# Optimization experiments

Measured on AMD Instinct MI355X. Metric: run time of the kernel, lower is better.

## Reference

```python
import jax, jax.numpy as jnp
import numpy as np
from jax import lax

B, TZ, TT = 16, 2048, 512
D, DFF, L, V, HEADS = 256, 1024, 6, 512, 4
CH, HID, K, FLOWS, G = 256, 256, 5, 4, 256
PAD_ID = 0
NEG = -1e9
SCALE = 0.02


def setup_inputs():
    key = jax.random.key(0)
    ks = jax.random.split(key, 20)
    n = lambda i, shape, s=SCALE: jax.random.normal(ks[i], shape, jnp.float32) * s
    return {
        'z': jax.random.normal(ks[0], (B, TZ, CH), jnp.float32),
        'text': jax.random.randint(ks[1], (B, TT), 1, V),  # low=1 so no pad tokens
        'cond': jax.random.normal(ks[2], (B, G), jnp.float32),
        'embed': n(3, (V, D), 1.0),
        'wq': n(4, (L, D, D)), 'wk': n(5, (L, D, D)), 'wv': n(6, (L, D, D)), 'wo': n(7, (L, D, D)),
        'bq': jnp.zeros((L, D)), 'bk': jnp.zeros((L, D)), 'bv': jnp.zeros((L, D)), 'bo': jnp.zeros((L, D)),
        'ln1_g': jnp.ones((L, D)), 'ln1_b': jnp.zeros((L, D)),
        'ln2_g': jnp.ones((L, D)), 'ln2_b': jnp.zeros((L, D)),
        'w1': n(8, (L, D, DFF)), 'b1': jnp.zeros((L, DFF)),
        'w2': n(9, (L, DFF, D)), 'b2': jnp.zeros((L, D)),
        'mu_w': n(10, (D, D)), 'mu_b': jnp.zeros((D,)),
        'lv_w': n(11, (D, D)), 'lv_b': jnp.zeros((D,)),
        'flow_in': n(12, (FLOWS, CH // 2, HID)), 'flow_in_b': jnp.zeros((FLOWS, HID)),
        'flow_cond': n(13, (FLOWS, G, HID)),
        'flow_conv': n(14, (FLOWS, K, HID, HID)), 'flow_conv_b': jnp.zeros((FLOWS, HID)),
        'flow_out': n(15, (FLOWS, HID, CH // 2)), 'flow_out_b': jnp.zeros((FLOWS, CH // 2)),
    }


def _pos_encoding(length, d):
    pos = np.arange(length)[:, None].astype(np.float32)
    i = np.arange(d)[None, :]
    angle = pos / np.power(10000.0, (2 * (i // 2)) / d)
    pe = np.where(i % 2 == 0, np.sin(angle), np.cos(angle))
    return jnp.asarray(pe, jnp.float32)


def _ln(x, g, b):
    m = jnp.mean(x, -1, keepdims=True)
    v = jnp.var(x, -1, keepdims=True)
    return g * (x - m) * lax.rsqrt(v + 1e-6) + b


def _mha(x, wq, wk, wv, wo, bq, bk, bv, bo, bias):
    Bq, T, _ = x.shape
    dh = D // HEADS
    heads = lambda y: y.reshape(Bq, T, HEADS, dh).transpose(0, 2, 1, 3)
    q, k, v = heads(x @ wq + bq), heads(x @ wk + bk), heads(x @ wv + bv)
    scores = jnp.einsum('bhqd,bhkd->bhqk', q, k) / jnp.sqrt(jnp.float32(dh)) + bias
    attn = jax.nn.softmax(scores, axis=-1)
    out = jnp.einsum('bhqk,bhkd->bhqd', attn, v).transpose(0, 2, 1, 3).reshape(Bq, T, D)
    return out @ wo + bo


def _mas_path(logp, text_mask):
    # Viterbi monotonic alignment: each latent frame t maps to text index j(t),
    # j nondecreasing with steps in {0, 1}, start at 0, end at last valid token.
    Bq, Tz, Tt = logp.shape
    Q0 = jnp.where(jnp.arange(Tt) == 0, logp[:, 0, :], NEG)

    def fwd(Q, lt):
        Qs = jnp.concatenate([jnp.full((Bq, 1), NEG, Q.dtype), Q[:, :-1]], axis=1)
        return lt + jnp.maximum(Q, Qs), Qs > Q  # choice True => came from j-1

    _, choices = lax.scan(fwd, Q0, jnp.swapaxes(logp, 0, 1)[1:])  # [Tz-1,B,Tt]
    j_last = jnp.sum(text_mask, axis=1).astype(jnp.int32) - 1

    def bwd(j, ch):
        c = jnp.take_along_axis(ch, j[:, None], axis=1)[:, 0]
        jp = j - c.astype(jnp.int32)
        return jp, jp

    _, path_rev = lax.scan(bwd, j_last, choices[::-1])
    path = jnp.concatenate([path_rev[::-1], j_last[None]], axis=0)  # [Tz,B]
    return jnp.swapaxes(path, 0, 1)


def _forward(z, text, cond, embed, wq, wk, wv, wo, bq, bk, bv, bo, ln1_g, ln1_b, ln2_g, ln2_b,
             w1, b1, w2, b2, mu_w, mu_b, lv_w, lv_b,
             flow_in, flow_in_b, flow_cond, flow_conv, flow_conv_b, flow_out, flow_out_b):
    text_mask = text != PAD_ID  # [B,TT]
    bias = jnp.where(text_mask[:, None, None, :], 0.0, NEG)
    # text encoder: scaled embedding + sinusoidal PE + post-LN transformer blocks
    h = embed[text] * jnp.sqrt(jnp.float32(D)) + _pos_encoding(TT, D)[None]
    for l in range(L):
        h = _ln(h + _mha(h, wq[l], wk[l], wv[l], wo[l], bq[l], bk[l], bv[l], bo[l], bias), ln1_g[l], ln1_b[l])
        ffn = jax.nn.relu(h @ w1[l] + b1[l]) @ w2[l] + b2[l]
        h = _ln(h + ffn, ln2_g[l], ln2_b[l])
    mu = h @ mu_w + mu_b
    logvar = h @ lv_w + lv_b
    # residual coupling flows (mean-only, conditioned on global vector)
    zc = z
    for f in range(FLOWS):
        x0, x1 = jnp.split(zc, 2, axis=-1)
        hh = x0 @ flow_in[f] + flow_in_b[f] + (cond @ flow_cond[f])[:, None, :]
        hh = jnp.tanh(lax.conv_general_dilated(hh, flow_conv[f], (1,), 'SAME', rhs_dilation=(1,),
                                               dimension_numbers=('NWC', 'WIO', 'NWC')) + flow_conv_b[f])
        m = hh @ flow_out[f] + flow_out_b[f]
        zc = jnp.concatenate([x1 + m, x0], axis=-1)  # coupling + flip
    # gaussian log-likelihood between latent frames and text distributions
    spr = jnp.exp(-logvar)  # [B,TT,D]
    nc1 = jnp.sum(-0.5 * jnp.log(2.0 * jnp.pi) - 0.5 * logvar, axis=-1)  # [B,TT]
    nc2 = jnp.einsum('btd,bjd->btj', -0.5 * zc * zc, spr)
    nc3 = jnp.einsum('btd,bjd->btj', zc, mu * spr)
    nc4 = jnp.sum(-0.5 * mu * mu * spr, axis=-1)  # [B,TT]
    logp = nc1[:, None, :] + nc2 + nc3 + nc4[:, None, :]  # [B,TZ,TT]
    logp = jnp.where(text_mask[:, None, :], logp, NEG)
    path = _mas_path(logp, text_mask)  # [B,TZ] int32
    ctx = mu[jnp.arange(B)[:, None], path]  # expand text mu along latent time
    return ctx, h


def reference(z, text, cond, embed, wq, wk, wv, wo, bq, bk, bv, bo, ln1_g, ln1_b, ln2_g, ln2_b,
              w1, b1, w2, b2, mu_w, mu_b, lv_w, lv_b,
              flow_in, flow_in_b, flow_cond, flow_conv, flow_conv_b, flow_out, flow_out_b):
    return _forward(z, text, cond, embed, wq, wk, wv, wo, bq, bk, bv, bo, ln1_g, ln1_b, ln2_g, ln2_b,
                    w1, b1, w2, b2, mu_w, mu_b, lv_w, lv_b,
                    flow_in, flow_in_b, flow_cond, flow_conv, flow_conv_b, flow_out, flow_out_b)
```

## Files before the change

kernel.cpp:

```cpp
#include <hip/hip_runtime.h>

#define BB 16
#define TZ_ 2048
#define TT_ 512
#define D_ 256
#define DFF_ 1024
#define L_ 6
#define HEADS_ 4
#define DH_ 64
#define CH_ 256
#define HID_ 256
#define KCV 5
#define FLOWS_ 4
#define G_ 256
#define NEGF (-1000000000.0f)
#define LOG2PI 1.8378770664093453f

typedef unsigned short u16;
typedef __attribute__((ext_vector_type(8))) short short8v;
typedef __attribute__((ext_vector_type(4))) float f32x4;
typedef __attribute__((ext_vector_type(4))) float f4v;
typedef __attribute__((ext_vector_type(4))) unsigned u4v;

__device__ __forceinline__ float wsum(float v){
#pragma unroll
  for (int o = 32; o; o >>= 1) v += __shfl_xor(v, o);
  return v;
}
__device__ __forceinline__ u16 f2bf(float x){
  unsigned u = __float_as_uint(x);
  return (u16)((u + 0x7FFFu + ((u >> 16) & 1u)) >> 16);
}
__device__ __forceinline__ float bf2f(u16 h){
  return __uint_as_float(((unsigned)h) << 16);
}
__device__ __forceinline__ unsigned pk2f(float a, float b){
  return __builtin_amdgcn_perm(__float_as_uint(b), __float_as_uint(a), 0x07060302u);
}
__device__ __forceinline__ float trnc(float f){
  return __uint_as_float(__float_as_uint(f) & 0xFFFF0000u);
}
__device__ __forceinline__ void cvt8t(float4 x, float4 y, uint4 &hi, uint4 &lo){
  hi.x = pk2f(x.x, x.y); hi.y = pk2f(x.z, x.w);
  hi.z = pk2f(y.x, y.y); hi.w = pk2f(y.z, y.w);
  float r0 = x.x - trnc(x.x), r1 = x.y - trnc(x.y), r2 = x.z - trnc(x.z), r3 = x.w - trnc(x.w);
  float r4 = y.x - trnc(y.x), r5 = y.y - trnc(y.y), r6 = y.z - trnc(y.z), r7 = y.w - trnc(y.w);
  lo.x = pk2f(r0, r1); lo.y = pk2f(r2, r3); lo.z = pk2f(r4, r5); lo.w = pk2f(r6, r7);
}
__device__ __forceinline__ unsigned rneh(float f){
  unsigned v = __float_as_uint(f);
  return (v + 0x7FFFu + ((v >> 16) & 1u)) & 0xFFFF0000u;
}
__device__ __forceinline__ void cvt8r(float4 x, float4 y, uint4 &hi, uint4 &lo){
  unsigned h0=rneh(x.x), h1=rneh(x.y), h2=rneh(x.z), h3=rneh(x.w);
  unsigned h4=rneh(y.x), h5=rneh(y.y), h6=rneh(y.z), h7=rneh(y.w);
  hi.x = h1 | (h0>>16); hi.y = h3 | (h2>>16); hi.z = h5 | (h4>>16); hi.w = h7 | (h6>>16);
  float r0 = x.x - __uint_as_float(h0), r1 = x.y - __uint_as_float(h1);
  float r2 = x.z - __uint_as_float(h2), r3 = x.w - __uint_as_float(h3);
  float r4 = y.x - __uint_as_float(h4), r5 = y.y - __uint_as_float(h5);
  float r6 = y.z - __uint_as_float(h6), r7 = y.w - __uint_as_float(h7);
  lo.x = pk2f(r0, r1); lo.y = pk2f(r2, r3); lo.z = pk2f(r4, r5); lo.w = pk2f(r6, r7);
}

__global__ void k_pe(float* __restrict__ pe){
  int t = blockIdx.x, d = threadIdx.x;
  double e = (double)(2*(d>>1)) / (double)D_;
  double ang = (double)t * pow(10000.0, -e);
  pe[t*D_ + d] = (float)(((d&1)==0) ? sin(ang) : cos(ang));
}
__global__ void k_embed(const int* __restrict__ text, const float* __restrict__ emb,
                        const float* __restrict__ pe, float* __restrict__ h){
  int row = blockIdx.x, d = threadIdx.x;
  h[(size_t)row*D_ + d] = emb[(size_t)text[row]*D_ + d]*16.0f + pe[(row%TT_)*D_ + d];
}

__global__ __launch_bounds__(256) void k_wt(
  const float* __restrict__ wq, const float* __restrict__ wk,
  const float* __restrict__ wv, const float* __restrict__ wo,
  const float* __restrict__ mu_w, const float* __restrict__ lv_w,
  const float* __restrict__ w1, const float* __restrict__ w2,
  float* __restrict__ QKVT, float* __restrict__ OT, float* __restrict__ MULVT,
  float* __restrict__ W1T, float* __restrict__ W2T)
{
  __shared__ float td[64][65];
  const int s = blockIdx.y, tile = blockIdx.x, t = threadIdx.x;
  const float* inb; float* outb; int istride, ostride;
  if (s < 24){
    int l = s>>2, wsel = s&3;
    const float* w = (wsel==0?wq:wsel==1?wk:wsel==2?wv:wo);
    inb = w + (size_t)l*65536; istride = 256;
    if (wsel < 3) outb = QKVT + (size_t)l*196608 + wsel*65536;
    else          outb = OT   + (size_t)l*65536;
    ostride = 256;
  } else if (s < 26){
    inb = (s==24 ? mu_w : lv_w); istride = 256;
    outb = MULVT + (size_t)(s-24)*65536; ostride = 256;
  } else if (s < 50){
    int idx = s-26, l = idx>>2, b2 = idx&3;
    inb = w1 + (size_t)l*262144 + b2*256; istride = 1024;
    outb = W1T + (size_t)l*262144 + (size_t)b2*65536; ostride = 256;
  } else {
    int idx = s-50, l = idx>>2, b2 = idx&3;
    inb = w2 + (size_t)l*262144 + (size_t)b2*65536; istride = 256;
    outb = W2T + (size_t)l*262144 + b2*256; ostride = 1024;
  }
  const int kt = (tile>>2)*64, nt = (tile&3)*64;
  const int r = t>>2, cq = (t&3)*16;
#pragma unroll
  for (int c=0;c<16;c+=4){
    float4 v = *(const float4*)(inb + (size_t)(kt + r)*istride + nt + cq + c);
    td[r][cq+c+0]=v.x; td[r][cq+c+1]=v.y; td[r][cq+c+2]=v.z; td[r][cq+c+3]=v.w;
  }
  __syncthreads();
#pragma unroll
  for (int c=0;c<16;c+=4){
    float4 v = make_float4(td[cq+c+0][r], td[cq+c+1][r], td[cq+c+2][r], td[cq+c+3][r]);
    *(float4*)(outb + (size_t)(nt + r)*ostride + kt + cq + c) = v;
  }
}

__global__ __launch_bounds__(256) void k_vt(const float* __restrict__ QKV, float* __restrict__ VT){
  __shared__ float td[64][65];
  const int b = blockIdx.z, dt = blockIdx.x, jt = blockIdx.y, t = threadIdx.x;
  const float* inb = QKV + (size_t)b*512*768 + 512;
  float* outb = VT + (size_t)b*131072;
  const int r = t>>2, cq = (t&3)*16;
#pragma unroll
  for (int c=0;c<16;c+=4){
    float4 v = *(const float4*)(inb + (size_t)(jt*64 + r)*768 + dt*64 + cq + c);
    td[r][cq+c+0]=v.x; td[r][cq+c+1]=v.y; td[r][cq+c+2]=v.z; td[r][cq+c+3]=v.w;
  }
  __syncthreads();
#pragma unroll
  for (int c=0;c<16;c+=4){
    float4 v = make_float4(td[cq+c+0][r], td[cq+c+1][r], td[cq+c+2][r], td[cq+c+3][r]);
    *(float4*)(outb + (size_t)(dt*64 + r)*512 + jt*64 + cq + c) = v;
  }
}

__global__ void k_bcat(const float* __restrict__ bq, const float* __restrict__ bk,
                       const float* __restrict__ bv, const float* __restrict__ mu_b,
                       const float* __restrict__ lv_b,
                       float* __restrict__ BQKV, float* __restrict__ MULVB){
  int i = blockIdx.x*256 + threadIdx.x;
  if (i < 4608){
    int l = i/768, c = i%768;
    float v = c<256 ? bq[l*256+c] : (c<512 ? bk[l*256+c-256] : bv[l*256+c-512]);
    BQKV[i] = v;
  } else if (i < 5120){
    int c = i-4608;
    MULVB[c] = c<256 ? mu_b[c] : lv_b[c-256];
  }
}

template<int WN, int EPI, int AM, int BMD>
__global__ __launch_bounds__(256,2) void k_mg(
  const void* __restrict__ Ap, const void* __restrict__ ApL, int lda, int azhi, int azlo,
  const void* __restrict__ Bp, const void* __restrict__ BpL, int ldb, int bzhi, int bzlo,
  const float* __restrict__ bias, const int* __restrict__ text,
  const float* __restrict__ nc1v, const float* __restrict__ nc4v,
  float* __restrict__ C, int ldc, int czhi, int czlo, int K)
{
  constexpr int BN = WN*32;
  __shared__ u16 AH[4096], AL[4096];
  __shared__ u16 BH[BN*32], BL[BN*32];
  char* AHB=(char*)AH; char* ALB=(char*)AL; char* BHB=(char*)BH; char* BLB=(char*)BL;
  const int t = threadIdx.x, z = blockIdx.z;
  const int m0 = blockIdx.y*128, n0 = blockIdx.x*BN;
  const size_t aoff = (size_t)(z>>2)*azhi + (size_t)(z&3)*azlo;
  const size_t boff = (size_t)(z>>2)*bzhi + (size_t)(z&3)*bzlo;
  const size_t coff = (size_t)(z>>2)*czhi + (size_t)(z&3)*czlo;
  const int w = t>>6, l = t&63;
  const int wr = (w>>1)*64, wc = (w&1)*(WN*16);
  const int lr = l&15, lg = l>>4;
  const int srow = t>>1, sseg = t&1;
  const int q  = (srow>>1)&3;
  const int wo0 = srow*64 + ((((sseg<<1)|0)^q)<<4);
  const int wo1 = srow*64 + ((((sseg<<1)|1)^q)<<4);
  const bool bact = (WN==4) || (t < 128);
  const int qa = ((wr+lr)>>1)&3, qb2 = ((wc+lr)>>1)&3;
  const int raBase = (wr+lr)*64 + ((lg^qa)<<4);
  const int rbBase = (wc+lr)*64 + ((lg^qb2)<<4);

  const float* Af = nullptr; const u16* AfH = nullptr; const u16* AfL = nullptr;
  if constexpr (AM==0 || AM==2){ Af = (const float*)Ap + aoff; }
  else { AfH = (const u16*)Ap + aoff; AfL = (const u16*)ApL + aoff; }
  const float* Bf = nullptr; const u16* BfH = nullptr; const u16* BfL = nullptr;
  if constexpr (BMD==0){ Bf = (const float*)Bp + boff; }
  else { BfH = (const u16*)Bp + boff; BfL = (const u16*)BpL + boff; }

  float4 sa0, sa1, sa2, sa3;
  uint4  pah0, pah1, pal0, pal1;
  float4 sb0, sb1, sb2, sb3;
  uint4  pbh0, pbh1, pbl0, pbl1;

  auto LOADA = [&](int kk){
    if constexpr (AM==0){
      const float* p = Af + (size_t)(m0+srow)*lda + kk + sseg*16;
      sa0=*(const float4*)p; sa1=*(const float4*)(p+4);
      sa2=*(const float4*)(p+8); sa3=*(const float4*)(p+12);
    } else if constexpr (AM==1){
      const u16* ph = AfH + (size_t)(m0+srow)*lda + kk + sseg*16;
      const u16* pl = AfL + (size_t)(m0+srow)*lda + kk + sseg*16;
      pah0 = *(const uint4*)ph; pah1 = *(const uint4*)(ph+8);
      pal0 = *(const uint4*)pl; pal1 = *(const uint4*)(pl+8);
    } else {
      int kg = kk + sseg*16;
      const float* p = Af + (size_t)(m0+srow)*lda + (kg < 256 ? kg : kg - 256);
      sa0=*(const float4*)p; sa1=*(const float4*)(p+4);
      sa2=*(const float4*)(p+8); sa3=*(const float4*)(p+12);
    }
  };
  auto LOADB = [&](int kk){
    if constexpr (BMD==0){
      const float* p = Bf + (size_t)(n0+srow)*ldb + kk + sseg*16;
      sb0=*(const float4*)p; sb1=*(const float4*)(p+4);
      sb2=*(const float4*)(p+8); sb3=*(const float4*)(p+12);
    } else {
      const u16* ph = BfH + (size_t)(n0+srow)*ldb + kk + sseg*16;
      const u16* pl = BfL + (size_t)(n0+srow)*ldb + kk + sseg*16;
      pbh0 = *(const uint4*)ph; pbh1 = *(const uint4*)(ph+8);
      pbl0 = *(const uint4*)pl; pbl1 = *(const uint4*)(pl+8);
    }
  };
  auto WRITEA = [&](int kk){
    uint4 ahi0, ahi1, alo0, alo1;
    if constexpr (AM==0){
      cvt8t(sa0,sa1,ahi0,alo0); cvt8t(sa2,sa3,ahi1,alo1);
    } else if constexpr (AM==1){
      ahi0=pah0; ahi1=pah1; alo0=pal0; alo1=pal1;
    } else {
      float4 a0=sa0, a1=sa1, a2=sa2, a3=sa3;
      int kg = kk + sseg*16;
      if (kg >= 256){
        a0.x=-0.5f*a0.x*a0.x; a0.y=-0.5f*a0.y*a0.y; a0.z=-0.5f*a0.z*a0.z; a0.w=-0.5f*a0.w*a0.w;
        a1.x=-0.5f*a1.x*a1.x; a1.y=-0.5f*a1.y*a1.y; a1.z=-0.5f*a1.z*a1.z; a1.w=-0.5f*a1.w*a1.w;
        a2.x=-0.5f*a2.x*a2.x; a2.y=-0.5f*a2.y*a2.y; a2.z=-0.5f*a2.z*a2.z; a2.w=-0.5f*a2.w*a2.w;
        a3.x=-0.5f*a3.x*a3.x; a3.y=-0.5f*a3.y*a3.y; a3.z=-0.5f*a3.z*a3.z; a3.w=-0.5f*a3.w*a3.w;
      }
      cvt8r(a0,a1,ahi0,alo0); cvt8r(a2,a3,ahi1,alo1);
    }
    *(uint4*)(AHB + wo0) = ahi0;  *(uint4*)(AHB + wo1) = ahi1;
    *(uint4*)(ALB + wo0) = alo0;  *(uint4*)(ALB + wo1) = alo1;
  };
  auto WRITEB = [&](){
    uint4 bhi0, bhi1, blo0, blo1;
    if constexpr (BMD==0){
      cvt8t(sb0,sb1,bhi0,blo0); cvt8t(sb2,sb3,bhi1,blo1);
    } else {
      bhi0=pbh0; bhi1=pbh1; blo0=pbl0; blo1=pbl1;
    }
    *(uint4*)(BHB + wo0) = bhi0;  *(uint4*)(BHB + wo1) = bhi1;
    *(uint4*)(BLB + wo0) = blo0;  *(uint4*)(BLB + wo1) = blo1;
  };

  f32x4 acc[4][WN];
#pragma unroll
  for (int i=0;i<4;i++)
#pragma unroll
    for (int j=0;j<WN;j++) acc[i][j] = (f32x4){0.f,0.f,0.f,0.f};

  LOADA(0);
  if (bact) LOADB(0);
  for (int k0 = 0; k0 < K; k0 += 32){
    __syncthreads();
    WRITEA(k0);
    if (bact) WRITEB();
    if (k0 + 32 < K){ LOADA(k0+32); if (bact) LOADB(k0+32); }
    __syncthreads();
    short8v fah[4], fal[4], fbh[WN], fbl[WN];
#pragma unroll
    for (int i=0;i<4;i++){
      fah[i] = *(short8v*)(AHB + raBase + i*1024);
      fal[i] = *(short8v*)(ALB + raBase + i*1024);
    }
#pragma unroll
    for (int j=0;j<WN;j++){
      fbh[j] = *(short8v*)(BHB + rbBase + j*1024);
      fbl[j] = *(short8v*)(BLB + rbBase + j*1024);
    }
#pragma unroll
    for (int i=0;i<4;i++)
#pragma unroll
      for (int j=0;j<WN;j++){
        acc[i][j] = __builtin_amdgcn_mfma_f32_16x16x32_bf16(fah[i], fbh[j], acc[i][j], 0,0,0);
        acc[i][j] = __builtin_amdgcn_mfma_f32_16x16x32_bf16(fal[i], fbh[j], acc[i][j], 0,0,0);
        acc[i][j] = __builtin_amdgcn_mfma_f32_16x16x32_bf16(fah[i], fbl[j], acc[i][j], 0,0,0);
      }
  }

#pragma unroll
  for (int i=0;i<4;i++){
    int mm0 = m0 + wr + i*16 + (lg<<2);
#pragma unroll
    for (int j=0;j<WN;j++){
      int nn = n0 + wc + j*16 + lr;
      float bs = 0.f; float ncb = 0.f; bool msk = true;
      if (EPI==0 || EPI==1) bs = bias ? bias[nn] : 0.f;
      if (EPI==2) msk = (text[(z>>2)*TT_ + nn] != 0);
      if (EPI==3){ ncb = nc1v[z*TT_+nn] + nc4v[z*TT_+nn]; msk = (text[z*TT_+nn] != 0); }
      f32x4 v = acc[i][j];
#pragma unroll
      for (int r=0;r<4;r++){
        int m = mm0 + r;
        float x;
        if (EPI==0)      x = v[r] + bs;
        else if (EPI==1) x = fmaxf(v[r] + bs, 0.f);
        else if (EPI==2) x = v[r]*0.125f + (msk ? 0.f : NEGF);
        else             x = msk ? (v[r] + ncb) : NEGF;
        C[coff + (size_t)m*ldc + nn] = x;
      }
    }
  }
}

__global__ __launch_bounds__(256) void k_softmax(float* __restrict__ S){
  size_t row = (size_t)blockIdx.x*4 + (threadIdx.x >> 6);
  float* p = S + row*TT_;
  int ln = threadIdx.x & 63;
  float4 a = *(float4*)(p + ln*8);
  float4 b = *(float4*)(p + ln*8 + 4);
  float x[8] = {a.x,a.y,a.z,a.w,b.x,b.y,b.z,b.w};
  float m = x[0];
#pragma unroll
  for (int i=1;i<8;i++) m = fmaxf(m, x[i]);
#pragma unroll
  for (int o2=32;o2;o2>>=1) m = fmaxf(m, __shfl_xor(m, o2));
  float s = 0.f;
#pragma unroll
  for (int i=0;i<8;i++){ x[i] = expf(x[i]-m); s += x[i]; }
  s = wsum(s);
  float inv = 1.0f/s;
  *(float4*)(p + ln*8)     = make_float4(x[0]*inv, x[1]*inv, x[2]*inv, x[3]*inv);
  *(float4*)(p + ln*8 + 4) = make_float4(x[4]*inv, x[5]*inv, x[6]*inv, x[7]*inv);
}

__global__ __launch_bounds__(256) void k_lnres(const float* __restrict__ y,
  const float* __restrict__ g, const float* __restrict__ bb, float* __restrict__ h){
  size_t row = blockIdx.x; int d = threadIdx.x;
  float v = h[row*D_ + d] + y[row*D_ + d];
  float s = wsum(v), s2 = wsum(v*v);
  __shared__ float r1[4], r2[4];
  int w = d >> 6;
  if ((d & 63) == 0){ r1[w] = s; r2[w] = s2; }
  __syncthreads();
  s  = r1[0]+r1[1]+r1[2]+r1[3];
  s2 = r2[0]+r2[1]+r2[2]+r2[3];
  float mean = s * (1.0f/D_);
  float var  = s2 * (1.0f/D_) - mean*mean;
  float inv  = rsqrtf(var + 1e-6f);
  h[row*D_ + d] = g[d]*(v - mean)*inv + bb[d];
}

__global__ __launch_bounds__(256) void k_prep(const float* __restrict__ mulv,
  u16* __restrict__ b2h, u16* __restrict__ b2l,
  float* __restrict__ nc1, float* __restrict__ nc4){
  size_t row = blockIdx.x; int d = threadIdx.x;
  float m = mulv[row*512 + d];
  float lv = mulv[row*512 + 256 + d];
  float sp = expf(-lv);
  float ms = m*sp;
  float s1 = wsum(lv), s2 = wsum(m*ms);
  __shared__ float r1[4], r2[4];
  int w = d >> 6;
  if ((d&63)==0){ r1[w]=s1; r2[w]=s2; }
  __syncthreads();
  if (d == 0){
    nc1[row] = -0.5f*((float)D_*LOG2PI + (r1[0]+r1[1]+r1[2]+r1[3]));
    nc4[row] = -0.5f*(r2[0]+r2[1]+r2[2]+r2[3]);
  }
  unsigned hm = rneh(ms);
  b2h[row*512 + d] = (u16)(hm>>16);
  b2l[row*512 + d] = f2bf(ms - __uint_as_float(hm));
  unsigned hs = rneh(sp);
  b2h[row*512 + 256 + d] = (u16)(hs>>16);
  b2l[row*512 + 256 + d] = f2bf(sp - __uint_as_float(hs));
}

__global__ __launch_bounds__(256) void k_fprep(
  const float* __restrict__ win, const float* __restrict__ wconv, const float* __restrict__ wout,
  u16* __restrict__ WITH, u16* __restrict__ WITL,
  u16* __restrict__ WCTH, u16* __restrict__ WCTL,
  u16* __restrict__ WOTH, u16* __restrict__ WOTL,
  const float* __restrict__ zsrc, u16* __restrict__ xh, u16* __restrict__ xl,
  const float* __restrict__ cond, const float* __restrict__ fcw, float* __restrict__ condp)
{
  const int bid = blockIdx.x, t = threadIdx.x;
  if (bid < 1536){
    int i = bid*256 + t;
    float wv2; u16 *dh, *dl; int idx;
    if (i < 32768){
      int n = i >> 7, k = i & 127;
      wv2 = win[k*256 + n]; dh = WITH; dl = WITL; idx = i;
    } else if (i < 360448){
      int jj = i - 32768;
      int o = jj / 1280, r = jj - o*1280;
      wv2 = wconv[(size_t)r*256 + o]; dh = WCTH; dl = WCTL; idx = jj;
    } else {
      int jj = i - 360448;
      int o = jj >> 8, k = jj & 255;
      wv2 = wout[k*128 + o]; dh = WOTH; dl = WOTL; idx = jj;
    }
    u16 hh = f2bf(wv2);
    dh[idx] = hh;
    dl[idx] = f2bf(wv2 - bf2f(hh));
  } else if (bid < 3584){
    size_t i = ((size_t)(bid-1536)*256 + t) << 3;
    size_t m2 = i >> 7; int k = (int)(i & 127);
    const float* src = zsrc + m2*256 + k;
    float4 a = *(const float4*)src; float4 b2 = *(const float4*)(src+4);
    float vv[8] = {a.x,a.y,a.z,a.w,b2.x,b2.y,b2.z,b2.w};
    short8v oh, ol;
#pragma unroll
    for (int r=0;r<8;r++){
      u16 hh = f2bf(vv[r]);
      oh[r] = (short)hh;
      ol[r] = (short)f2bf(vv[r] - bf2f(hh));
    }
    *(short8v*)(xh + i) = oh;
    *(short8v*)(xl + i) = ol;
  } else {
    int b = bid - 3584, n = t;
    float s = 0.f;
    for (int k2=0;k2<G_;k2++) s = fmaf(cond[b*G_ + k2], fcw[k2*HID_ + n], s);
    condp[b*HID_ + n] = s;
  }
}

__global__ void k_padzero2(u16* __restrict__ XpH, u16* __restrict__ XpL){
  int i = blockIdx.x*256 + threadIdx.x;
  u16* P = (i >> 14) ? XpL : XpH;
  int ii = i & 16383;
  int b = ii >> 10, rr = (ii >> 8) & 3, c = ii & 255;
  int row = (rr < 2) ? rr : (2048 + rr);
  P[((size_t)b*2052 + row)*256 + c] = 0;
}

template<int EPI, int SPLITOUT>
__global__ __launch_bounds__(256,2) void k_mf2(
  const u16* __restrict__ Ah, const u16* __restrict__ Al, int lda, int padA,
  const u16* __restrict__ Bh, const u16* __restrict__ Bl, int ldb,
  const float* __restrict__ bias, const float* __restrict__ cnd,
  void* __restrict__ CH, void* __restrict__ CL, int ldc, int padC, int K)
{
  __shared__ u16 AsmH[4096], AsmL[4096], BsmH[4096], BsmL[4096];
  char* AHB=(char*)AsmH; char* ALB=(char*)AsmL;
  char* BHB=(char*)BsmH; char* BLB=(char*)BsmL;
  const int t = threadIdx.x;
  const int m0 = blockIdx.y << 7, n0 = blockIdx.x << 7;
  const int w = t >> 6, l = t & 63;
  const int wr = (w >> 1) << 6, wc = (w & 1) << 6;
  const int lr = l & 15, lg = l >> 4;
  const int srow = t >> 1, sseg = t & 1;
  const int q = (srow >> 1) & 3;
  const int wo0 = srow*64 + ((((sseg<<1)|0) ^ q) << 4);
  const int wo1 = srow*64 + ((((sseg<<1)|1) ^ q) << 4);
  const int am = m0 + srow;
  const size_t aoff = (size_t)(am + padA*(am >> 11))*lda + (sseg << 4);
  const u16* AhP = Ah + aoff;
  const u16* AlP = Al + aoff;
  const size_t boff = (size_t)(n0 + srow)*ldb + (sseg << 4);
  const u16* BhP = Bh + boff;
  const u16* BlP = Bl + boff;
  const int qa = ((wr + lr) >> 1) & 3, qb = ((wc + lr) >> 1) & 3;
  const int raBase = (wr + lr)*64 + ((lg ^ qa) << 4);
  const int rbBase = (wc + lr)*64 + ((lg ^ qb) << 4);
  f32x4 acc[4][4];
#pragma unroll
  for (int i=0;i<4;i++)
#pragma unroll
    for (int j=0;j<4;j++) acc[i][j] = (f32x4){0.f,0.f,0.f,0.f};

  float4 sah0, sah1, sal0, sal1, sbh0, sbh1, sbl0, sbl1;
  auto LOADF = [&](int kk){
    sah0 = *(const float4*)(AhP + kk); sah1 = *(const float4*)(AhP + kk + 8);
    sal0 = *(const float4*)(AlP + kk); sal1 = *(const float4*)(AlP + kk + 8);
    sbh0 = *(const float4*)(BhP + kk); sbh1 = *(const float4*)(BhP + kk + 8);
    sbl0 = *(const float4*)(BlP + kk); sbl1 = *(const float4*)(BlP + kk + 8);
  };

  LOADF(0);
  for (int k0 = 0; k0 < K; k0 += 32){
    __syncthreads();
    *(float4*)(AHB + wo0) = sah0;  *(float4*)(AHB + wo1) = sah1;
    *(float4*)(ALB + wo0) = sal0;  *(float4*)(ALB + wo1) = sal1;
    *(float4*)(BHB + wo0) = sbh0;  *(float4*)(BHB + wo1) = sbh1;
    *(float4*)(BLB + wo0) = sbl0;  *(float4*)(BLB + wo1) = sbl1;
    if (k0 + 32 < K) LOADF(k0 + 32);
    __syncthreads();
    short8v fah[4], fal[4], fbh[4], fbl[4];
#pragma unroll
    for (int i=0;i<4;i++){
      fah[i] = *(short8v*)(AHB + raBase + i*1024);
      fal[i] = *(short8v*)(ALB + raBase + i*1024);
    }
#pragma unroll
    for (int j=0;j<4;j++){
      fbh[j] = *(short8v*)(BHB + rbBase + j*1024);
      fbl[j] = *(short8v*)(BLB + rbBase + j*1024);
    }
#pragma unroll
    for (int i=0;i<4;i++)
#pragma unroll
      for (int j=0;j<4;j++){
        acc[i][j] = __builtin_amdgcn_mfma_f32_16x16x32_bf16(fah[i], fbh[j], acc[i][j], 0, 0, 0);
        acc[i][j] = __builtin_amdgcn_mfma_f32_16x16x32_bf16(fal[i], fbh[j], acc[i][j], 0, 0, 0);
        acc[i][j] = __builtin_amdgcn_mfma_f32_16x16x32_bf16(fah[i], fbl[j], acc[i][j], 0, 0, 0);
      }
  }

#pragma unroll
  for (int i=0;i<4;i++){
    int mbase = m0 + wr + i*16 + (lg << 2);
#pragma unroll
    for (int j=0;j<4;j++){
      int nn = n0 + wc + j*16 + lr;
      float bs = bias[nn];
      f32x4 v = acc[i][j];
#pragma unroll
      for (int r=0;r<4;r++){
        int m = mbase + r;
        float x = v[r] + bs;
        if (EPI == 1) x += cnd[((m >> 11) << 8) + nn];
        if (EPI == 2) x = tanhf(x);
        if (EPI == 3) x += cnd[(size_t)m*256 + 128 + nn];
        size_t ro = (size_t)(m + padC*(m >> 11))*ldc + nn;
        if (SPLITOUT){
          u16 xh = f2bf(x);
          ((u16*)CH)[ro] = xh;
          ((u16*)CL)[ro] = f2bf(x - bf2f(xh));
        } else {
          ((float*)CH)[ro] = x;
          if (EPI == 3)
            ((float*)CH)[(size_t)m*ldc + 128 + nn] = cnd[(size_t)m*256 + nn];
        }
      }
    }
  }
}

__device__ __forceinline__ void mas_row1(float4 u0, float4 u1, float* Q, int ln, int tr,
                                         unsigned char* __restrict__ cb){
  float v[8] = {u0.x,u0.y,u0.z,u0.w,u1.x,u1.y,u1.z,u1.w};
  float qp = __shfl_up(Q[7], 1);
  if (ln == 0) qp = NEGF;
  unsigned bits = 0; float qs = qp;
#pragma unroll
  for (int i=0;i<8;i++){
    float old = Q[i];
    if (qs > old) bits |= (1u<<i);
    Q[i] = v[i] + fmaxf(old, qs);
    qs = old;
  }
  cb[(size_t)(tr-1)*64 + ln] = (unsigned char)bits;
}

__global__ __launch_bounds__(64,1) void k_mas(const float* __restrict__ lp,
  const int* __restrict__ text, unsigned char* __restrict__ cho, int* __restrict__ path)
{
  const int b = blockIdx.x, ln = threadIdx.x;
  const float* L = lp + (size_t)b*TZ_*TT_;
  const float* Lr = L + ln*8;
  unsigned char* cb = cho + (size_t)b*TZ_*64;
  __shared__ __align__(16) unsigned char lch[3*4096];

  float Q[8];
#pragma unroll
  for (int i=0;i<8;i++) Q[i] = NEGF;
  if (ln == 0) Q[0] = L[0];

  float4 P0a = *(const float4*)(Lr + (size_t)1*TT_), P0b = *(const float4*)(Lr + (size_t)1*TT_ + 4);
  float4 P1a = *(const float4*)(Lr + (size_t)2*TT_), P1b = *(const float4*)(Lr + (size_t)2*TT_ + 4);
  float4 P2a = *(const float4*)(Lr + (size_t)3*TT_), P2b = *(const float4*)(Lr + (size_t)3*TT_ + 4);
  float4 P3a = *(const float4*)(Lr + (size_t)4*TT_), P3b = *(const float4*)(Lr + (size_t)4*TT_ + 4);
  float4 P4a = *(const float4*)(Lr + (size_t)5*TT_), P4b = *(const float4*)(Lr + (size_t)5*TT_ + 4);
  float4 P5a = *(const float4*)(Lr + (size_t)6*TT_), P5b = *(const float4*)(Lr + (size_t)6*TT_ + 4);
  float4 P6a = *(const float4*)(Lr + (size_t)7*TT_), P6b = *(const float4*)(Lr + (size_t)7*TT_ + 4);
  float4 P7a = *(const float4*)(Lr + (size_t)8*TT_), P7b = *(const float4*)(Lr + (size_t)8*TT_ + 4);
  asm volatile("" ::: "memory");

  int t0 = 1;
#define MAS_SLOT(Pa, Pb, OFF) \
    mas_row1(Pa, Pb, Q, ln, t0 + OFF, cb); \
    { const float* _s = Lr + (size_t)(t0 + OFF + 8)*TT_; \
      Pa = *(const float4*)_s; Pb = *(const float4*)(_s + 4); } \
    asm volatile("" ::: "memory");
  for (; t0 + 15 <= TZ_ - 1; t0 += 8){
    MAS_SLOT(P0a, P0b, 0)
    MAS_SLOT(P1a, P1b, 1)
    MAS_SLOT(P2a, P2b, 2)
    MAS_SLOT(P3a, P3b, 3)
    MAS_SLOT(P4a, P4b, 4)
    MAS_SLOT(P5a, P5b, 5)
    MAS_SLOT(P6a, P6b, 6)
    MAS_SLOT(P7a, P7b, 7)
  }
#undef MAS_SLOT
  mas_row1(P0a,P0b,Q,ln,t0+0,cb);
  mas_row1(P1a,P1b,Q,ln,t0+1,cb);
  mas_row1(P2a,P2b,Q,ln,t0+2,cb);
  mas_row1(P3a,P3b,Q,ln,t0+3,cb);
  mas_row1(P4a,P4b,Q,ln,t0+4,cb);
  mas_row1(P5a,P5b,Q,ln,t0+5,cb);
  mas_row1(P6a,P6b,Q,ln,t0+6,cb);
  mas_row1(P7a,P7b,Q,ln,t0+7,cb);
  for (int t = t0 + 8; t < TZ_; t++){
    const float* s = Lr + (size_t)t*TT_;
    float4 a = *(const float4*)s;
    float4 c = *(const float4*)(s + 4);
    mas_row1(a, c, Q, ln, t, cb);
  }

  int cnt = 0;
#pragma unroll
  for (int i=0;i<8;i++) cnt += (text[b*TT_ + ln*8 + i] != 0) ? 1 : 0;
#pragma unroll
  for (int o2=32;o2;o2>>=1) cnt += __shfl_xor(cnt, o2);
  const int jl = cnt - 1;
  if (ln == 0) path[b*TZ_ + TZ_-1] = jl;

  __syncthreads();

  const int NP = TZ_ - 1;
  uint* lchU = (uint*)lch;
  const uint* cbU = (const uint*)cb;
  {
    int r0 = 2046 - ln;
#pragma unroll
    for (int k=0;k<4;k++)
      *(u4v*)&lchU[0*1024 + ln*16 + k*4] = *(const u4v*)&cbU[(size_t)r0*16 + k*4];
    int r1 = 2046 - (64 + ln);
#pragma unroll
    for (int k=0;k<4;k++)
      *(u4v*)&lchU[1*1024 + ln*16 + k*4] = *(const u4v*)&cbU[(size_t)r1*16 + k*4];
  }
  u4v su0, su1, su2, su3;
  {
    int r2 = 2046 - (128 + ln);
    su0 = *(const u4v*)&cbU[(size_t)r2*16 + 0];
    su1 = *(const u4v*)&cbU[(size_t)r2*16 + 4];
    su2 = *(const u4v*)&cbU[(size_t)r2*16 + 8];
    su3 = *(const u4v*)&cbU[(size_t)r2*16 + 12];
  }

  int j = jl;
  unsigned rb0[8], rb1[8]; int rc[8];
  if (ln == 0){
#pragma unroll
    for (int qd=0; qd<8; qd++){
      int cHi = jl >> 3;
      int cLo = (cHi > 0) ? cHi - 1 : 0;
      rb1[qd] = lch[qd*64 + cHi];
      rb0[qd] = lch[qd*64 + cLo];
      rc[qd]  = cHi;
    }
  }
  for (int H = 0; H < 32; H++){
    if (H + 2 < 32){
      uint* wb = lchU + ((H+2)%3)*1024;
      *(u4v*)&wb[ln*16 + 0]  = su0;
      *(u4v*)&wb[ln*16 + 4]  = su1;
      *(u4v*)&wb[ln*16 + 8]  = su2;
      *(u4v*)&wb[ln*16 + 12] = su3;
    }
    if (H + 3 < 32){
      int p = (H+3)*64 + ln;
      if (p <= 2046){
        int r = 2046 - p;
        su0 = *(const u4v*)&cbU[(size_t)r*16 + 0];
        su1 = *(const u4v*)&cbU[(size_t)r*16 + 4];
        su2 = *(const u4v*)&cbU[(size_t)r*16 + 8];
        su3 = *(const u4v*)&cbU[(size_t)r*16 + 12];
      }
    }
    if (ln == 0){
      int pbase = H*64;
#pragma unroll 8
      for (int s = 0; s < 64; s++){
        int p = pbase + s;
        if (p < NP){
          int r = s & 7;
          int jb = j >> 3;
          unsigned byte = (jb == rc[r]) ? rb1[r] : rb0[r];
          j -= (int)((byte >> (j & 7)) & 1u);
          path[b*TZ_ + 2046 - p] = j;
          int pn = p + 8;
          if (pn < NP){
            int hn = (pn >> 6) % 3, sn = pn & 63;
            int cHi = j >> 3;
            int cLo = (cHi > 0) ? cHi - 1 : 0;
            rb1[r] = lch[hn*4096 + sn*64 + cHi];
            rb0[r] = lch[hn*4096 + sn*64 + cLo];
            rc[r]  = cHi;
          }
        }
      }
    }
    __syncthreads();
  }
}

__global__ void k_gather(const float* __restrict__ mulv, const int* __restrict__ path,
  const float* __restrict__ h, float* __restrict__ out){
  size_t i = (size_t)blockIdx.x*256 + threadIdx.x;
  const size_t N4 = (size_t)BB*TZ_*(D_/4);
  const size_t H4 = (size_t)BB*TT_*(D_/4);
  if (i < N4){
    size_t row = i >> 6; int c = (int)(i & 63);
    int b = (int)(row >> 11);
    int pj = path[row];
    ((float4*)out)[i] = *(const float4*)(mulv + ((size_t)b*TT_ + pj)*512 + (size_t)c*4);
  } else if (i < N4 + H4){
    size_t k2 = i - N4;
    ((float4*)out)[i] = ((const float4*)h)[k2];
  }
}

extern "C" void kernel_launch(void* const* d_in, const int* in_sizes, int n_in,
                              void* d_out, int out_size, void* d_ws, size_t ws_size,
                              hipStream_t stream)
{
  (void)in_sizes; (void)n_in; (void)out_size; (void)ws_size;
  const float* z      = (const float*)d_in[0];
  const int*   text   = (const int*)  d_in[1];
  const float* cond   = (const float*)d_in[2];
  const float* emb    = (const float*)d_in[3];
  const float* wq     = (const float*)d_in[4];
  const float* wk     = (const float*)d_in[5];
  const float* wv     = (const float*)d_in[6];
  const float* wo     = (const float*)d_in[7];
  const float* bq     = (const float*)d_in[8];
  const float* bk     = (const float*)d_in[9];
  const float* bv     = (const float*)d_in[10];
  const float* bo     = (const float*)d_in[11];
  const float* ln1g   = (const float*)d_in[12];
  const float* ln1b   = (const float*)d_in[13];
  const float* ln2g   = (const float*)d_in[14];
  const float* ln2b   = (const float*)d_in[15];
  const float* w1     = (const float*)d_in[16];
  const float* b1     = (const float*)d_in[17];
  const float* w2     = (const float*)d_in[18];
  const float* b2     = (const float*)d_in[19];
  const float* mu_w   = (const float*)d_in[20];
  const float* mu_b   = (const float*)d_in[21];
  const float* lv_w   = (const float*)d_in[22];
  const float* lv_b   = (const float*)d_in[23];
  const float* f_in   = (const float*)d_in[24];
  const float* f_in_b = (const float*)d_in[25];
  const float* f_cond = (const float*)d_in[26];
  const float* f_conv = (const float*)d_in[27];
  const float* f_convb= (const float*)d_in[28];
  const float* f_out  = (const float*)d_in[29];
  const float* f_outb = (const float*)d_in[30];

  float* ws = (float*)d_ws;
  size_t o = 0;
  float* PE   = ws + o; o += (size_t)131072;
  float* H    = ws + o; o += (size_t)2097152;
  float* MULV = ws + o; o += (size_t)4194304;
  float* NC1  = ws + o; o += (size_t)8192;
  float* NC4  = ws + o; o += (size_t)8192;
  float* CONDP= ws + o; o += (size_t)4096;
  int*   PATH = (int*)(ws + o); o += (size_t)32768;
  u16*  B2H  = (u16*)(ws + o); o += (size_t)2097152;
  u16*  B2L  = (u16*)(ws + o); o += (size_t)2097152;
  float* BIGS = ws + o; o += (size_t)16777216;
  float* BUF1 = ws + o; o += (size_t)4587520;
  float* BUF2 = ws + o; o += (size_t)10485760;
  float* ZCA  = ws + o; o += (size_t)8388608;
  float* ZCB  = ws + o; o += (size_t)8388608;

  float* QKV = BUF2;
  float* Yb  = QKV + 6291456;
  float* VT  = Yb + 2097152;
  float* ATTO= QKV;
  float* QKVT = ZCA;
  float* OT   = QKVT + 1179648;
  float* W1T  = OT + 393216;
  float* W2T  = W1T + 1572864;
  float* MULVT= W2T + 1572864;
  float* BQKV = MULVT + 131072;
  float* MULVB= BQKV + 4608;
  u16*  X0H = (u16*)BUF1;
  u16*  X0L = X0H + 4194304;
  u16*  WITH = X0L + 4194304;
  u16*  WITL = WITH + 32768;
  u16*  WCTH = WITL + 32768;
  u16*  WCTL = WCTH + 327680;
  u16*  WOTH = WCTL + 327680;
  u16*  WOTL = WOTH + 32768;
  u16*  XpH = (u16*)BIGS;
  u16*  XpL = XpH + 8404992;
  u16*  H2H = (u16*)BUF2;
  u16*  H2L = H2H + 8388608;
  unsigned char* CHO = (unsigned char*)ZCA;

  k_pe   <<<dim3(TT_),    dim3(D_), 0, stream>>>(PE);
  k_embed<<<dim3(BB*TT_), dim3(D_), 0, stream>>>(text, emb, PE, H);
  k_wt   <<<dim3(16,74), 256, 0, stream>>>(wq,wk,wv,wo,mu_w,lv_w,w1,w2, QKVT,OT,MULVT,W1T,W2T);
  k_bcat <<<dim3(20), 256, 0, stream>>>(bq,bk,bv,mu_b,lv_b, BQKV, MULVB);

  for (int l=0;l<L_;l++){
    k_mg<4,0,0,0><<<dim3(6,64,1),256,0,stream>>>(
      H, nullptr, 256, 0,0,  QKVT + (size_t)l*196608, nullptr, 256, 0,0,
      BQKV + l*768, nullptr, nullptr, nullptr, QKV, 768, 0,0, 256);
    k_vt <<<dim3(4,8,16),256,0,stream>>>(QKV, VT);
    k_mg<4,2,0,0><<<dim3(4,4,64),256,0,stream>>>(
      QKV, nullptr, 768, 393216, 64,  QKV+256, nullptr, 768, 393216, 64,
      nullptr, text, nullptr, nullptr, BIGS, 512, 1048576, 262144, 64);
    k_softmax<<<dim3(BB*HEADS_*TT_/4),256,0,stream>>>(BIGS);
    k_mg<2,0,0,0><<<dim3(1,4,64),256,0,stream>>>(
      BIGS, nullptr, 512, 1048576, 262144,  VT, nullptr, 512, 131072, 32768,
      nullptr, nullptr, nullptr, nullptr, Yb, 256, 131072, 64, 512);
    k_mg<4,0,0,0><<<dim3(2,64,1),256,0,stream>>>(
      Yb, nullptr, 256, 0,0,  OT + (size_t)l*65536, nullptr, 256, 0,0,
      bo + l*256, nullptr, nullptr, nullptr, ATTO, 256, 0,0, 256);
    k_lnres<<<dim3(BB*TT_),256,0,stream>>>(ATTO, ln1g+l*D_, ln1b+l*D_, H);
    k_mg<4,1,0,0><<<dim3(8,64,1),256,0,stream>>>(
      H, nullptr, 256, 0,0,  W1T + (size_t)l*262144, nullptr, 256, 0,0,
      b1 + l*1024, nullptr, nullptr, nullptr, BIGS, 1024, 0,0, 256);
    k_mg<4,0,0,0><<<dim3(2,64,1),256,0,stream>>>(
      BIGS, nullptr, 1024, 0,0,  W2T + (size_t)l*262144, nullptr, 1024, 0,0,
      b2 + l*256, nullptr, nullptr, nullptr, ATTO, 256, 0,0, 1024);
    k_lnres<<<dim3(BB*TT_),256,0,stream>>>(ATTO, ln2g+l*D_, ln2b+l*D_, H);
  }

  k_mg<4,0,0,0><<<dim3(4,64,1),256,0,stream>>>(
    H, nullptr, 256, 0,0,  MULVT, nullptr, 256, 0,0,
    MULVB, nullptr, nullptr, nullptr, MULV, 512, 0,0, 256);
  k_prep<<<dim3(BB*TT_),256,0,stream>>>(MULV, B2H, B2L, NC1, NC4);

  k_padzero2<<<dim3(128),256,0,stream>>>(XpH, XpL);
  const float* zsrc = z;
  for (int f=0; f<FLOWS_; f++){
    k_fprep<<<dim3(3600),256,0,stream>>>(
        f_in + (size_t)f*(CH_/2)*HID_, f_conv + (size_t)f*KCV*HID_*HID_,
        f_out + (size_t)f*HID_*(CH_/2),
        WITH, WITL, WCTH, WCTL, WOTH, WOTL,
        zsrc, X0H, X0L,
        cond, f_cond + (size_t)f*G_*HID_, CONDP);
    k_mf2<1,1><<<dim3(2,256),256,0,stream>>>(X0H, X0L, 128, 0, WITH, WITL, 128,
        f_in_b + f*HID_, CONDP, (void*)(XpH + 512), (void*)(XpL + 512), 256, 4, 128);
    k_mf2<2,1><<<dim3(2,256),256,0,stream>>>(XpH, XpL, 256, 4, WCTH, WCTL, 1280,
        f_convb + f*HID_, nullptr, (void*)H2H, (void*)H2L, 256, 0, 1280);
    float* zdst = (f & 1) ? ZCB : ZCA;
    k_mf2<3,0><<<dim3(1,256),256,0,stream>>>(H2H, H2L, 256, 0, WOTH, WOTL, 256,
        f_outb + f*(CH_/2), zsrc, (void*)zdst, nullptr, 256, 0, 256);
    zsrc = zdst;
  }

  k_mg<4,3,2,1><<<dim3(4,16,16),256,0,stream>>>(
    zsrc, nullptr, 256, 2097152, 524288,
    B2H, B2L, 512, 1048576, 262144,
    nullptr, text, NC1, NC4, BIGS, 512, 4194304, 1048576, 512);

  k_mas<<<dim3(BB),64,0,stream>>>(BIGS, text, CHO, PATH);
  k_gather<<<dim3((BB*TZ_*D_/4 + BB*TT_*D_/4)/256),256,0,stream>>>(MULV, PATH, H, (float*)d_out);
}
```

Measured before the change: 2.191 ms.

## Fuse softmax normalization into the attention PV GEMM A-operand load

```diff
diff --git a/kernel.cpp b/kernel.cpp
--- a/kernel.cpp
+++ b/kernel.cpp
@@ -19,7 +19,6 @@
 typedef unsigned short u16;
 typedef __attribute__((ext_vector_type(8))) short short8v;
 typedef __attribute__((ext_vector_type(4))) float f32x4;
-typedef __attribute__((ext_vector_type(4))) float f4v;
 typedef __attribute__((ext_vector_type(4))) unsigned u4v;
 
 __device__ __forceinline__ float wsum(float v){
@@ -183,19 +182,26 @@
   const int rbBase = (wc+lr)*64 + ((lg^qb2)<<4);
 
   const float* Af = nullptr; const u16* AfH = nullptr; const u16* AfL = nullptr;
-  if constexpr (AM==0 || AM==2){ Af = (const float*)Ap + aoff; }
+  if constexpr (AM==0 || AM==2 || AM==4){ Af = (const float*)Ap + aoff; }
   else { AfH = (const u16*)Ap + aoff; AfL = (const u16*)ApL + aoff; }
   const float* Bf = nullptr; const u16* BfH = nullptr; const u16* BfL = nullptr;
   if constexpr (BMD==0){ Bf = (const float*)Bp + boff; }
   else { BfH = (const u16*)Bp + boff; BfL = (const u16*)BpL + boff; }
 
+  float mrow = 0.f, sinv = 0.f;
+  if constexpr (AM==4){
+    int rg = z*TT_ + m0 + srow;
+    mrow = nc1v[rg];
+    sinv = nc4v[rg];
+  }
+
   float4 sa0, sa1, sa2, sa3;
   uint4  pah0, pah1, pal0, pal1;
   float4 sb0, sb1, sb2, sb3;
   uint4  pbh0, pbh1, pbl0, pbl1;
 
   auto LOADA = [&](int kk){
-    if constexpr (AM==0){
+    if constexpr (AM==0 || AM==4){
       const float* p = Af + (size_t)(m0+srow)*lda + kk + sseg*16;
       sa0=*(const float4*)p; sa1=*(const float4*)(p+4);
       sa2=*(const float4*)(p+8); sa3=*(const float4*)(p+12);
@@ -227,6 +233,13 @@
     uint4 ahi0, ahi1, alo0, alo1;
     if constexpr (AM==0){
       cvt8t(sa0,sa1,ahi0,alo0); cvt8t(sa2,sa3,ahi1,alo1);
+    } else if constexpr (AM==4){
+      float4 a0=sa0, a1=sa1, a2=sa2, a3=sa3;
+      a0.x=expf(a0.x-mrow)*sinv; a0.y=expf(a0.y-mrow)*sinv; a0.z=expf(a0.z-mrow)*sinv; a0.w=expf(a0.w-mrow)*sinv;
+      a1.x=expf(a1.x-mrow)*sinv; a1.y=expf(a1.y-mrow)*sinv; a1.z=expf(a1.z-mrow)*sinv; a1.w=expf(a1.w-mrow)*sinv;
+      a2.x=expf(a2.x-mrow)*sinv; a2.y=expf(a2.y-mrow)*sinv; a2.z=expf(a2.z-mrow)*sinv; a2.w=expf(a2.w-mrow)*sinv;
+      a3.x=expf(a3.x-mrow)*sinv; a3.y=expf(a3.y-mrow)*sinv; a3.z=expf(a3.z-mrow)*sinv; a3.w=expf(a3.w-mrow)*sinv;
+      cvt8t(a0,a1,ahi0,alo0); cvt8t(a2,a3,ahi1,alo1);
     } else if constexpr (AM==1){
       ahi0=pah0; ahi1=pah1; alo0=pal0; alo1=pal1;
     } else {
@@ -314,12 +327,13 @@
   }
 }
 
-__global__ __launch_bounds__(256) void k_softmax(float* __restrict__ S){
+__global__ __launch_bounds__(256) void k_rowstat(const float* __restrict__ S,
+  float* __restrict__ MR, float* __restrict__ SR){
   size_t row = (size_t)blockIdx.x*4 + (threadIdx.x >> 6);
-  float* p = S + row*TT_;
+  const float* p = S + row*TT_;
   int ln = threadIdx.x & 63;
-  float4 a = *(float4*)(p + ln*8);
-  float4 b = *(float4*)(p + ln*8 + 4);
+  float4 a = *(const float4*)(p + ln*8);
+  float4 b = *(const float4*)(p + ln*8 + 4);
   float x[8] = {a.x,a.y,a.z,a.w,b.x,b.y,b.z,b.w};
   float m = x[0];
 #pragma unroll
@@ -328,11 +342,12 @@
   for (int o2=32;o2;o2>>=1) m = fmaxf(m, __shfl_xor(m, o2));
   float s = 0.f;
 #pragma unroll
-  for (int i=0;i<8;i++){ x[i] = expf(x[i]-m); s += x[i]; }
+  for (int i=0;i<8;i++){ s += expf(x[i]-m); }
   s = wsum(s);
-  float inv = 1.0f/s;
-  *(float4*)(p + ln*8)     = make_float4(x[0]*inv, x[1]*inv, x[2]*inv, x[3]*inv);
-  *(float4*)(p + ln*8 + 4) = make_float4(x[4]*inv, x[5]*inv, x[6]*inv, x[7]*inv);
+  if (ln == 0){
+    MR[row] = m;
+    SR[row] = 1.0f/s;
+  }
 }
 
 __global__ __launch_bounds__(256) void k_lnres(const float* __restrict__ y,
@@ -760,6 +775,8 @@
   float* MULV = ws + o; o += (size_t)4194304;
   float* NC1  = ws + o; o += (size_t)8192;
   float* NC4  = ws + o; o += (size_t)8192;
+  float* MR   = ws + o; o += (size_t)32768;
+  float* SR   = ws + o; o += (size_t)32768;
   float* CONDP= ws + o; o += (size_t)4096;
   int*   PATH = (int*)(ws + o); o += (size_t)32768;
   u16*  B2H  = (u16*)(ws + o); o += (size_t)2097152;
@@ -808,10 +825,10 @@
     k_mg<4,2,0,0><<<dim3(4,4,64),256,0,stream>>>(
       QKV, nullptr, 768, 393216, 64,  QKV+256, nullptr, 768, 393216, 64,
       nullptr, text, nullptr, nullptr, BIGS, 512, 1048576, 262144, 64);
-    k_softmax<<<dim3(BB*HEADS_*TT_/4),256,0,stream>>>(BIGS);
-    k_mg<2,0,0,0><<<dim3(1,4,64),256,0,stream>>>(
+    k_rowstat<<<dim3(BB*HEADS_*TT_/4),256,0,stream>>>(BIGS, MR, SR);
+    k_mg<2,0,4,0><<<dim3(1,4,64),256,0,stream>>>(
       BIGS, nullptr, 512, 1048576, 262144,  VT, nullptr, 512, 131072, 32768,
-      nullptr, nullptr, nullptr, nullptr, Yb, 256, 131072, 64, 512);
+      nullptr, nullptr, MR, SR, Yb, 256, 131072, 64, 512);
     k_mg<4,0,0,0><<<dim3(2,64,1),256,0,stream>>>(
       Yb, nullptr, 256, 0,0,  OT + (size_t)l*65536, nullptr, 256, 0,0,
       bo + l*256, nullptr, nullptr, nullptr, ATTO, 256, 0,0, 256);
```

After: 2.157 ms (median of 2 runs). No clear change (-1.5%).
